# Kernel optimization log

Measured on AMD Instinct MI355X. Metric: run time of the kernel, lower is better.

The kernel has to match this reference:

```python
import jax, jax.numpy as jnp
import numpy as np

IN_DIM = 4096
UNITS = 4096
BATCH = 4096
SIGMA_INIT = 0.5


def _scale_noise(key, size):
    x = jax.random.normal(key, (size,), dtype=jnp.float32)
    return jnp.sign(x) * jnp.sqrt(jnp.abs(x))


def setup_inputs() -> dict:
    key = jax.random.key(0)
    kx, kwmu, kbmu, kein, keout = jax.random.split(key, 5)
    bound = 1.0 / np.sqrt(IN_DIM)
    x = jax.random.normal(kx, (BATCH, IN_DIM), dtype=jnp.float32)
    w_mu = jax.random.uniform(kwmu, (IN_DIM, UNITS), minval=-bound, maxval=bound, dtype=jnp.float32)
    w_sigma = jnp.full((IN_DIM, UNITS), SIGMA_INIT * bound, dtype=jnp.float32)
    b_mu = jax.random.uniform(kbmu, (UNITS,), minval=-bound, maxval=bound, dtype=jnp.float32)
    b_sigma = jnp.full((UNITS,), SIGMA_INIT * bound, dtype=jnp.float32)
    eps_in = _scale_noise(kein, IN_DIM)
    eps_out = _scale_noise(keout, UNITS)
    return {"x": x, "w_mu": w_mu, "w_sigma": w_sigma, "b_mu": b_mu,
            "b_sigma": b_sigma, "eps_in": eps_in, "eps_out": eps_out}


def reference(x, w_mu, w_sigma, b_mu, b_sigma, eps_in, eps_out):
    # training-mode NoisyDense: w = w_mu + w_sigma * outer(eps_in, eps_out)
    eps_w = eps_in[:, None] * eps_out[None, :]        # [IN_DIM, UNITS]
    w = w_mu + w_sigma * eps_w
    b = b_mu + b_sigma * eps_out
    out = jnp.matmul(x, w) + b                         # [BATCH, UNITS]
    return jax.nn.relu(out)
```

## Files before the change

kernel.cpp:

```cpp
#include <hip/hip_runtime.h>
#include <hip/hip_bf16.h>
#include <stdint.h>

#define M_DIM 4096
#define K_DIM 4096
#define N_DIM 4096

typedef __bf16 bf16_t;
typedef __bf16  bf16x8 __attribute__((ext_vector_type(8)));
typedef float   f32x4  __attribute__((ext_vector_type(4)));
typedef float   floatx4 __attribute__((ext_vector_type(4)));

__device__ __forceinline__ void gload_lds16(const bf16_t* g, bf16_t* l) {
    __builtin_amdgcn_global_load_lds(
        (const __attribute__((address_space(1))) void*)(uintptr_t)g,
        (__attribute__((address_space(3))) void*)(uintptr_t)(unsigned)(uintptr_t)l,
        16, 0, 0);
}

__global__ __launch_bounds__(256) void convert_x(const float* __restrict__ x,
                                                 bf16_t* __restrict__ xb) {
    size_t idx = (size_t)blockIdx.x * blockDim.x + threadIdx.x;
    const floatx4* x4 = (const floatx4*)x;
    floatx4 a = x4[idx * 2];
    floatx4 b = x4[idx * 2 + 1];
    bf16x8 o;
    o[0] = (bf16_t)a[0]; o[1] = (bf16_t)a[1]; o[2] = (bf16_t)a[2]; o[3] = (bf16_t)a[3];
    o[4] = (bf16_t)b[0]; o[5] = (bf16_t)b[1]; o[6] = (bf16_t)b[2]; o[7] = (bf16_t)b[3];
    *(bf16x8*)&xb[idx * 8] = o;
}

__global__ __launch_bounds__(256) void build_wt(const float* __restrict__ w_mu,
                                                const float* __restrict__ w_sigma,
                                                const float* __restrict__ eps_in,
                                                const float* __restrict__ eps_out,
                                                bf16_t* __restrict__ wt) {
    __shared__ float tile[64][65];
    int bk = blockIdx.x & 63;
    int bn = blockIdx.x >> 6;
    int k0 = bk * 64, n0 = bn * 64;
    int t = threadIdx.x;
    int c = t & 63;
    float eo = eps_out[n0 + c];
#pragma unroll
    for (int p = 0; p < 16; ++p) {
        int r = p * 4 + (t >> 6);
        int k = k0 + r;
        float ei = eps_in[k];
        size_t off = (size_t)k * N_DIM + n0 + c;
        tile[r][c] = w_mu[off] + w_sigma[off] * (ei * eo);
    }
    __syncthreads();
#pragma unroll
    for (int p = 0; p < 8; ++p) {
        int rn = p * 8 + (t >> 5);
        int ck = (t & 31) * 2;
        bf16_t v0 = (bf16_t)tile[ck][rn];
        bf16_t v1 = (bf16_t)tile[ck + 1][rn];
        union { bf16_t b[2]; unsigned u; } u2;
        u2.b[0] = v0; u2.b[1] = v1;
        *(unsigned*)&wt[(size_t)(n0 + rn) * K_DIM + k0 + ck] = u2.u;
    }
}

#define BM 256
#define BN 256
#define BK 64
#define NT (K_DIM / BK)

__device__ __forceinline__ void stage_half(bf16_t* lds, const bf16_t* g, int kcol0, int t) {
#pragma unroll
    for (int p = 0; p < 2; ++p) {
        int chunk = p * 512 + t;
        int row = chunk >> 3;
        int c16 = chunk & 7;
        gload_lds16(g + (size_t)row * K_DIM + kcol0 + ((c16 ^ (row & 7)) << 3),
                    lds + row * BK + (c16 << 3));
    }
}

__device__ __forceinline__ bf16x8 lds_frag(const bf16_t* base, int row, int kcol) {
    int c16 = kcol >> 3;
    return *(const bf16x8*)(base + row * BK + (((c16 ^ (row & 7)) << 3)));
}

#define BAR()  asm volatile("s_barrier" ::: "memory")
#define VM0()  asm volatile("s_waitcnt vmcnt(0)" ::: "memory")

__global__ __launch_bounds__(512, 2) void gemm8p(
    const bf16_t* __restrict__ A,
    const bf16_t* __restrict__ Bt,
    const float* __restrict__ b_mu,
    const float* __restrict__ b_sigma,
    const float* __restrict__ eps_out,
    float* __restrict__ C) {

    __shared__ __align__(16) bf16_t As[2][BM * BK];
    __shared__ __align__(16) bf16_t Bs[2][BN * BK];

    int bid = blockIdx.x;
    int swz = (bid & 7) * (gridDim.x >> 3) + (bid >> 3);
    int tm = swz & 15, tn = swz >> 4;
    size_t bm = (size_t)tm * BM, bn = (size_t)tn * BN;

    int t = threadIdx.x;
    int lane = t & 63;
    int wave = t >> 6;
    int wr = wave >> 2, wc = wave & 3;
    int l15 = lane & 15;
    int kseg = (lane >> 4) << 3;

    const bf16_t* Ab = A  + bm * (size_t)K_DIM;
    const bf16_t* Bb = Bt + bn * (size_t)K_DIM;

    f32x4 zero = {0.f, 0.f, 0.f, 0.f};
    f32x4 acc[8][4];
#pragma unroll
    for (int i = 0; i < 8; ++i)
#pragma unroll
        for (int j = 0; j < 4; ++j) acc[i][j] = zero;

    stage_half(&As[0][0],            Ab,                        0, t);
    stage_half(&As[0][128 * BK],     Ab + (size_t)128 * K_DIM,  0, t);
    stage_half(&Bs[0][0],            Bb,                        0, t);
    stage_half(&Bs[0][128 * BK],     Bb + (size_t)128 * K_DIM,  0, t);
    VM0();
    BAR();

    for (int kt = 0; kt < NT; ++kt) {
        const int cur = kt & 1, nxt = cur ^ 1;
        const bf16_t* As_c = &As[cur][0];
        const bf16_t* Bs_c = &Bs[cur][0];
        const int kb1 = (kt + 1) * BK;
        const bool st1 = (kt + 1 < NT);
        bf16x8 af[4][2], bq0[2][2], bq1[2][2];

#pragma unroll
        for (int mi = 0; mi < 4; ++mi)
#pragma unroll
            for (int kk = 0; kk < 2; ++kk)
                af[mi][kk] = lds_frag(As_c, wr * 128 + mi * 16 + l15, kk * 32 + kseg);
#pragma unroll
        for (int ni = 0; ni < 2; ++ni)
#pragma unroll
            for (int kk = 0; kk < 2; ++kk)
                bq0[ni][kk] = lds_frag(Bs_c, wc * 64 + ni * 16 + l15, kk * 32 + kseg);
        if (st1) {
            stage_half(&As[nxt][0],        Ab,                       kb1, t);
            stage_half(&As[nxt][128 * BK], Ab + (size_t)128 * K_DIM, kb1, t);
            stage_half(&Bs[nxt][0],        Bb,                       kb1, t);
            stage_half(&Bs[nxt][128 * BK], Bb + (size_t)128 * K_DIM, kb1, t);
        }
        BAR();
        __builtin_amdgcn_s_setprio(1);
#pragma unroll
        for (int mi = 0; mi < 4; ++mi)
#pragma unroll
            for (int ni = 0; ni < 2; ++ni)
#pragma unroll
                for (int kk = 0; kk < 2; ++kk)
                    acc[mi][ni] = __builtin_amdgcn_mfma_f32_16x16x32_bf16(
                        af[mi][kk], bq0[ni][kk], acc[mi][ni], 0, 0, 0);
        __builtin_amdgcn_s_setprio(0);
        BAR();

#pragma unroll
        for (int ni = 0; ni < 2; ++ni)
#pragma unroll
            for (int kk = 0; kk < 2; ++kk)
                bq1[ni][kk] = lds_frag(Bs_c, wc * 64 + 32 + ni * 16 + l15, kk * 32 + kseg);
        BAR();
        __builtin_amdgcn_s_setprio(1);
#pragma unroll
        for (int mi = 0; mi < 4; ++mi)
#pragma unroll
            for (int ni = 0; ni < 2; ++ni)
#pragma unroll
                for (int kk = 0; kk < 2; ++kk)
                    acc[mi][2 + ni] = __builtin_amdgcn_mfma_f32_16x16x32_bf16(
                        af[mi][kk], bq1[ni][kk], acc[mi][2 + ni], 0, 0, 0);
        __builtin_amdgcn_s_setprio(0);
        BAR();

#pragma unroll
        for (int mi = 0; mi < 4; ++mi)
#pragma unroll
            for (int kk = 0; kk < 2; ++kk)
                af[mi][kk] = lds_frag(As_c, wr * 128 + 64 + mi * 16 + l15, kk * 32 + kseg);
        BAR();
        __builtin_amdgcn_s_setprio(1);
#pragma unroll
        for (int mi = 0; mi < 4; ++mi)
#pragma unroll
            for (int ni = 0; ni < 2; ++ni)
#pragma unroll
                for (int kk = 0; kk < 2; ++kk)
                    acc[4 + mi][2 + ni] = __builtin_amdgcn_mfma_f32_16x16x32_bf16(
                        af[mi][kk], bq1[ni][kk], acc[4 + mi][2 + ni], 0, 0, 0);
        __builtin_amdgcn_s_setprio(0);
        BAR();

        __builtin_amdgcn_s_setprio(1);
#pragma unroll
        for (int mi = 0; mi < 4; ++mi)
#pragma unroll
            for (int ni = 0; ni < 2; ++ni)
#pragma unroll
                for (int kk = 0; kk < 2; ++kk)
                    acc[4 + mi][ni] = __builtin_amdgcn_mfma_f32_16x16x32_bf16(
                        af[mi][kk], bq0[ni][kk], acc[4 + mi][ni], 0, 0, 0);
        __builtin_amdgcn_s_setprio(0);
        VM0();
        BAR();
    }

    int col0 = l15;
    int row0 = (lane >> 4) * 4;
#pragma unroll
    for (int qn = 0; qn < 2; ++qn)
#pragma unroll
        for (int ni = 0; ni < 2; ++ni) {
            int n = (int)bn + wc * 64 + qn * 32 + ni * 16 + col0;
            float bias = b_mu[n] + b_sigma[n] * eps_out[n];
#pragma unroll
            for (int qm = 0; qm < 2; ++qm)
#pragma unroll
                for (int mi = 0; mi < 4; ++mi) {
                    int m = (int)bm + wr * 128 + qm * 64 + mi * 16 + row0;
                    f32x4 v = acc[qm * 4 + mi][qn * 2 + ni];
#pragma unroll
                    for (int r = 0; r < 4; ++r) {
                        float o = v[r] + bias;
                        C[(size_t)(m + r) * N_DIM + n] = o > 0.f ? o : 0.f;
                    }
                }
        }
}

extern "C" void kernel_launch(void* const* d_in, const int* in_sizes, int n_in,
                              void* d_out, int out_size, void* d_ws, size_t ws_size,
                              hipStream_t stream) {
    const float* x       = (const float*)d_in[0];
    const float* w_mu    = (const float*)d_in[1];
    const float* w_sigma = (const float*)d_in[2];
    const float* b_mu    = (const float*)d_in[3];
    const float* b_sigma = (const float*)d_in[4];
    const float* eps_in  = (const float*)d_in[5];
    const float* eps_out = (const float*)d_in[6];
    float* out = (float*)d_out;

    bf16_t* xb = (bf16_t*)d_ws;
    bf16_t* wt = (bf16_t*)((char*)d_ws + (size_t)M_DIM * K_DIM * 2);

    convert_x<<<(M_DIM * K_DIM) / (8 * 256), 256, 0, stream>>>(x, xb);
    build_wt<<<64 * 64, 256, 0, stream>>>(w_mu, w_sigma, eps_in, eps_out, wt);
    gemm8p<<<(M_DIM / BM) * (N_DIM / BN), 512, 0, stream>>>(
        xb, wt, b_mu, b_sigma, eps_out, out);
}
```

Measured before the change: 179.1 us.

## Interleave next-tile global loads across MFMA phases with partial vmcnt waits

Splits the next-tile A/B staging into four quarter-sized load groups (interleaved row sets matching each wave's consumption), issued one per compute phase instead of all at the top of the iteration. Uses partial vmcnt waits and sched_barrier fences so loads stay in flight across MFMA blocks rather than draining fully each iteration. The aim is to hide global-to-LDS latency better and smooth memory issue, at the cost of more barriers and fragile waitcnt accounting that must match the interleaved row mapping.

```diff
diff --git a/kernel.cpp b/kernel.cpp
--- a/kernel.cpp
+++ b/kernel.cpp
@@ -68,24 +68,40 @@
 #define BK 64
 #define NT (K_DIM / BK)
 
-__device__ __forceinline__ void stage_half(bf16_t* lds, const bf16_t* g, int kcol0, int t) {
+__device__ __forceinline__ void stage_Aset(bf16_t* lds, const bf16_t* g, int kcol0, int t, int off) {
 #pragma unroll
     for (int p = 0; p < 2; ++p) {
         int chunk = p * 512 + t;
-        int row = chunk >> 3;
+        int r = chunk >> 3;
+        int row = ((r >> 6) << 7) + (r & 63) + off;
         int c16 = chunk & 7;
         gload_lds16(g + (size_t)row * K_DIM + kcol0 + ((c16 ^ (row & 7)) << 3),
                     lds + row * BK + (c16 << 3));
     }
 }
 
+__device__ __forceinline__ void stage_Bset(bf16_t* lds, const bf16_t* g, int kcol0, int t, int off) {
+#pragma unroll
+    for (int p = 0; p < 2; ++p) {
+        int chunk = p * 512 + t;
+        int r = chunk >> 3;
+        int row = ((r >> 5) << 6) + (r & 31) + off;
+        int c16 = chunk & 7;
+        gload_lds16(g + (size_t)row * K_DIM + kcol0 + ((c16 ^ (row & 7)) << 3),
+                    lds + row * BK + (c16 << 3));
+    }
+}
+
 __device__ __forceinline__ bf16x8 lds_frag(const bf16_t* base, int row, int kcol) {
     int c16 = kcol >> 3;
     return *(const bf16x8*)(base + row * BK + (((c16 ^ (row & 7)) << 3)));
 }
 
-#define BAR()  asm volatile("s_barrier" ::: "memory")
-#define VM0()  asm volatile("s_waitcnt vmcnt(0)" ::: "memory")
+#define BARB()   __builtin_amdgcn_s_barrier()
+#define SCHED0() __builtin_amdgcn_sched_barrier(0)
+#define LGKM0()  asm volatile("s_waitcnt lgkmcnt(0)")
+#define VMW2()   asm volatile("s_waitcnt vmcnt(2)")
+#define VMW0()   asm volatile("s_waitcnt vmcnt(0)")
 
 __global__ __launch_bounds__(512, 2) void gemm8p(
     const bf16_t* __restrict__ A,
@@ -120,17 +136,21 @@
 #pragma unroll
         for (int j = 0; j < 4; ++j) acc[i][j] = zero;
 
-    stage_half(&As[0][0],            Ab,                        0, t);
-    stage_half(&As[0][128 * BK],     Ab + (size_t)128 * K_DIM,  0, t);
-    stage_half(&Bs[0][0],            Bb,                        0, t);
-    stage_half(&Bs[0][128 * BK],     Bb + (size_t)128 * K_DIM,  0, t);
-    VM0();
-    BAR();
+    stage_Aset(&As[0][0], Ab, 0, t, 0);
+    stage_Aset(&As[0][0], Ab, 0, t, 64);
+    stage_Bset(&Bs[0][0], Bb, 0, t, 0);
+    stage_Bset(&Bs[0][0], Bb, 0, t, 32);
+    VMW0();
+    SCHED0();
+    BARB();
+    SCHED0();
 
     for (int kt = 0; kt < NT; ++kt) {
         const int cur = kt & 1, nxt = cur ^ 1;
         const bf16_t* As_c = &As[cur][0];
         const bf16_t* Bs_c = &Bs[cur][0];
+        bf16_t* As_n = &As[nxt][0];
+        bf16_t* Bs_n = &Bs[nxt][0];
         const int kb1 = (kt + 1) * BK;
         const bool st1 = (kt + 1 < NT);
         bf16x8 af[4][2], bq0[2][2], bq1[2][2];
@@ -145,13 +165,8 @@
 #pragma unroll
             for (int kk = 0; kk < 2; ++kk)
                 bq0[ni][kk] = lds_frag(Bs_c, wc * 64 + ni * 16 + l15, kk * 32 + kseg);
-        if (st1) {
-            stage_half(&As[nxt][0],        Ab,                       kb1, t);
-            stage_half(&As[nxt][128 * BK], Ab + (size_t)128 * K_DIM, kb1, t);
-            stage_half(&Bs[nxt][0],        Bb,                       kb1, t);
-            stage_half(&Bs[nxt][128 * BK], Bb + (size_t)128 * K_DIM, kb1, t);
-        }
-        BAR();
+        if (st1) stage_Aset(As_n, Ab, kb1, t, 0);
+        SCHED0(); BARB(); LGKM0(); SCHED0();
         __builtin_amdgcn_s_setprio(1);
 #pragma unroll
         for (int mi = 0; mi < 4; ++mi)
@@ -162,14 +177,16 @@
                     acc[mi][ni] = __builtin_amdgcn_mfma_f32_16x16x32_bf16(
                         af[mi][kk], bq0[ni][kk], acc[mi][ni], 0, 0, 0);
         __builtin_amdgcn_s_setprio(0);
-        BAR();
+        if (kt == NT - 1) { VMW0(); } else { VMW2(); }
+        SCHED0(); BARB(); SCHED0();
 
 #pragma unroll
         for (int ni = 0; ni < 2; ++ni)
 #pragma unroll
             for (int kk = 0; kk < 2; ++kk)
                 bq1[ni][kk] = lds_frag(Bs_c, wc * 64 + 32 + ni * 16 + l15, kk * 32 + kseg);
-        BAR();
+        if (st1) stage_Bset(Bs_n, Bb, kb1, t, 0);
+        SCHED0(); BARB(); LGKM0(); SCHED0();
         __builtin_amdgcn_s_setprio(1);
 #pragma unroll
         for (int mi = 0; mi < 4; ++mi)
@@ -180,14 +197,15 @@
                     acc[mi][2 + ni] = __builtin_amdgcn_mfma_f32_16x16x32_bf16(
                         af[mi][kk], bq1[ni][kk], acc[mi][2 + ni], 0, 0, 0);
         __builtin_amdgcn_s_setprio(0);
-        BAR();
+        SCHED0(); BARB(); SCHED0();
 
 #pragma unroll
         for (int mi = 0; mi < 4; ++mi)
 #pragma unroll
             for (int kk = 0; kk < 2; ++kk)
                 af[mi][kk] = lds_frag(As_c, wr * 128 + 64 + mi * 16 + l15, kk * 32 + kseg);
-        BAR();
+        if (st1) stage_Aset(As_n, Ab, kb1, t, 64);
+        SCHED0(); BARB(); LGKM0(); SCHED0();
         __builtin_amdgcn_s_setprio(1);
 #pragma unroll
         for (int mi = 0; mi < 4; ++mi)
@@ -198,8 +216,10 @@
                     acc[4 + mi][2 + ni] = __builtin_amdgcn_mfma_f32_16x16x32_bf16(
                         af[mi][kk], bq1[ni][kk], acc[4 + mi][2 + ni], 0, 0, 0);
         __builtin_amdgcn_s_setprio(0);
-        BAR();
-
+        SCHED0(); BARB(); SCHED0();
+
+        if (st1) stage_Bset(Bs_n, Bb, kb1, t, 32);
+        SCHED0(); BARB(); SCHED0();
         __builtin_amdgcn_s_setprio(1);
 #pragma unroll
         for (int mi = 0; mi < 4; ++mi)
@@ -210,8 +230,8 @@
                     acc[4 + mi][ni] = __builtin_amdgcn_mfma_f32_16x16x32_bf16(
                         af[mi][kk], bq0[ni][kk], acc[4 + mi][ni], 0, 0, 0);
         __builtin_amdgcn_s_setprio(0);
-        VM0();
-        BAR();
+        VMW2();
+        SCHED0(); BARB(); SCHED0();
     }
 
     int col0 = l15;
```

Result: faster. 171.6 us (median of 2 runs) (-4.2%).
